# Kernel tuning notes

Hardware: AMD Instinct MI355X
Metric: run time of the kernel (lower is better)

## Reference

```python
import jax, jax.numpy as jnp
import numpy as np

B, C, REP, H, W = 4, 256, 128, 32, 128
EPS = 1e-5


def _conv1x1(x, w, b=None):
    # x: [B, Cin, H, W], w: [Cout, Cin]
    y = jnp.einsum('oc,bchw->bohw', w, x)
    if b is not None:
        y = y + b[None, :, None, None]
    return y


def _bn_train(x, gamma, beta):
    # BatchNorm2d in training mode: batch stats over (B, H, W)
    mean = jnp.mean(x, axis=(0, 2, 3), keepdims=True)
    var = jnp.var(x, axis=(0, 2, 3), keepdims=True)
    xn = (x - mean) * jax.lax.rsqrt(var + EPS)
    return gamma[None, :, None, None] * xn + beta[None, :, None, None]


def setup_inputs() -> dict:
    key = jax.random.key(0)
    ks = jax.random.split(key, 20)
    f = lambda k, s: jax.random.normal(k, s, dtype=jnp.float32)
    inp = {
        'left': f(ks[0], (B, C, H, W)),
        'right': f(ks[1], (B, C, H, W)),
        'pre_l': jax.random.uniform(ks[2], (B, 1, H, W), dtype=jnp.float32) * W,
        'pre_r': jax.random.uniform(ks[3], (B, 1, H, W), dtype=jnp.float32) * W,
        'query_l': f(ks[4], (B, REP, H, W)),
        'key_l': f(ks[5], (B, REP, H, W)),
        'query_r': f(ks[6], (B, REP, H, W)),
        'key_r': f(ks[7], (B, REP, H, W)),
        # learned 1x1-conv params (kernel stored as [Cout, Cin])
        'theta_w': f(ks[8], (REP, C + 1)) * 0.02,
        'theta_b': f(ks[9], (REP,)) * 0.02,
        'phi_w': f(ks[10], (REP, C)) * 0.02,
        'phi_b': f(ks[11], (REP,)) * 0.02,
        'g_w': f(ks[12], (REP, C)) * 0.02,
        'g_b': f(ks[13], (REP,)) * 0.02,
        'up_w': f(ks[14], (C, REP)) * 0.02,
        'up_b': f(ks[15], (C,)) * 0.02,
        'bn_gamma': f(ks[16], (C,)) * 0.1 + 1.0,
        'bn_beta': f(ks[17], (C,)) * 0.1,
    }
    return inp


def _side(x_q, x_kv, pre, query, key_feat,
          theta_w, theta_b, phi_w, phi_b, g_w, g_b,
          up_w, up_b, bn_gamma, bn_beta):
    hw = H * W
    pre = pre / W
    # theta: [B, hw, REP]
    theta = _conv1x1(jnp.concatenate([x_q, pre], axis=1), theta_w, theta_b)
    theta = theta.reshape(B, REP, hw).transpose(0, 2, 1) + \
        query.reshape(B, REP, hw).transpose(0, 2, 1)
    # phi: [B, REP, hw]
    phi = _conv1x1(x_kv, phi_w, phi_b).reshape(B, REP, hw) + \
        key_feat.reshape(B, REP, hw)
    # g: [B, hw, REP]
    g = _conv1x1(x_kv, g_w, g_b).reshape(B, REP, hw).transpose(0, 2, 1)
    # attention over all hw key positions: [B, hw, hw]
    atten = jax.nn.softmax(jnp.einsum('bqc,bck->bqk', theta, phi), axis=-1)
    # soft-argmax over key column index (arange(W) tiled H times along key axis)
    col_idx = jnp.tile(jnp.arange(W, dtype=jnp.float32), H)  # [hw]
    exp_col = jnp.einsum('bqk,k->bq', atten, col_idx)        # [B, hw]
    q_col = (jnp.arange(hw, dtype=jnp.float32) % W)[None, :]  # [1, hw]
    index = (q_col - exp_col).reshape(B, H, W)
    # value aggregation + residual projection
    after = jnp.einsum('bqk,bkc->bqc', atten, g)
    after = after.transpose(0, 2, 1).reshape(B, REP, H, W)
    out = x_q + _bn_train(_conv1x1(after, up_w, up_b), bn_gamma, bn_beta)
    return out, index


def reference(left, right, pre_l, pre_r, query_l, key_l, query_r, key_r,
              theta_w, theta_b, phi_w, phi_b, g_w, g_b,
              up_w, up_b, bn_gamma, bn_beta):
    l_n, index_l = _side(left, right, pre_l, query_l, key_r,
                         theta_w, theta_b, phi_w, phi_b, g_w, g_b,
                         up_w, up_b, bn_gamma, bn_beta)
    r_n, index_r = _side(right, left, pre_r, query_r, key_l,
                         theta_w, theta_b, phi_w, phi_b, g_w, g_b,
                         up_w, up_b, bn_gamma, bn_beta)
    return (l_n, r_n, index_l, index_r)
```

## Files before the change

### kernel.cpp

```cpp
#include <hip/hip_runtime.h>


typedef unsigned short u16;
typedef unsigned int   u32;
typedef float        floatx4 __attribute__((ext_vector_type(4)));
typedef unsigned int uintx4  __attribute__((ext_vector_type(4)));
typedef unsigned int uintx2  __attribute__((ext_vector_type(2)));
typedef _Float16     half8   __attribute__((ext_vector_type(8)));
typedef __fp16       fp16x2  __attribute__((ext_vector_type(2)));

#define HW 4096
#define CB 256
#define RP 128
#define EPSF 1e-5f

static __device__ __forceinline__ u16 f2bf(float f) {
  u32 u = __float_as_uint(f);
  u32 r = u + 0x7FFFu + ((u >> 16) & 1u);
  return (u16)(r >> 16);
}
static __device__ __forceinline__ float bf2f(u16 h) {
  return __uint_as_float(((u32)h) << 16);
}
static __device__ __forceinline__ u16 f2h(float f) {
  _Float16 h = (_Float16)f;
  return __builtin_bit_cast(u16, h);
}
static __device__ __forceinline__ float h2f(u16 h) {
  return (float)__builtin_bit_cast(_Float16, h);
}
static __device__ __forceinline__ half8 as_h8(uintx4 v) {
  return __builtin_bit_cast(half8, v);
}
static __device__ __forceinline__ u32 pkrtz(float a, float b) {
  fp16x2 h = __builtin_amdgcn_cvt_pkrtz(a, b);
  return __builtin_bit_cast(u32, h);
}
static __device__ __forceinline__ u32 pk2h(float a, float b) {
  return (u32)f2h(a) | ((u32)f2h(b) << 16);
}
static __device__ __forceinline__ void barrier_nodrain() {
  __builtin_amdgcn_sched_barrier(0);
  asm volatile("s_waitcnt lgkmcnt(0)" ::: "memory");
  __builtin_amdgcn_s_barrier();
  __builtin_amdgcn_sched_barrier(0);
}

union Pk4 { u16 u[4]; uintx2 v; };

struct ProjCfg {
  const float* x; const float* w; const float* bias;
  const float* add; const float* pre; u16* out;
  int wstride; int transposed;
};
struct ProjCfg6 { ProjCfg c[6]; };

#define XSTR 40

__global__ __launch_bounds__(256) void ra_projm(ProjCfg6 cfg)
{
  __shared__ u16 x_lds[128 * XSTR];
  __shared__ u16 w_lds[128 * XSTR];
  const ProjCfg C = cfg.c[blockIdx.x >> 7];
  const int inner = blockIdx.x & 127;
  const int b    = inner >> 5;
  const int pos0 = (inner & 31) * 128;
  const int tid  = threadIdx.x;
  const int wv   = tid >> 6;
  const int lane = tid & 63;
  const int ln16 = lane & 15;
  const int quad = lane >> 4;
  const int mbase = wv * 32;

  const int xc0 = (tid & 7) * 4, xp0 = (tid >> 3) * 4;
  const int wrr = tid >> 1, wch = (tid & 1) * 16;

  floatx4 acc[2][8];
  #pragma unroll
  for (int mt = 0; mt < 2; mt++)
    #pragma unroll
    for (int nt = 0; nt < 8; nt++) acc[mt][nt] = (floatx4)0.0f;

  #pragma unroll 1
  for (int cc = 0; cc < 8; ++cc) {
    floatx4 xr[4];
    #pragma unroll
    for (int i = 0; i < 4; i++)
      xr[i] = *(const floatx4*)(C.x + (size_t)(b * CB + cc * 32 + xc0 + i) * HW + pos0 + xp0);
    float ww[16];
    {
      const float* wp = C.w + (size_t)wrr * C.wstride + cc * 32 + wch;
      #pragma unroll
      for (int i = 0; i < 16; i++) ww[i] = wp[i];
    }
    __syncthreads();
    #pragma unroll
    for (int pp = 0; pp < 4; pp++) {
      uintx2 v;
      v[0] = pk2h(xr[0][pp], xr[1][pp]);
      v[1] = pk2h(xr[2][pp], xr[3][pp]);
      *(uintx2*)&x_lds[(xp0 + pp) * XSTR + xc0] = v;
    }
    {
      uintx4 v0, v1;
      v0[0] = pk2h(ww[0], ww[1]);  v0[1] = pk2h(ww[2], ww[3]);
      v0[2] = pk2h(ww[4], ww[5]);  v0[3] = pk2h(ww[6], ww[7]);
      v1[0] = pk2h(ww[8], ww[9]);  v1[1] = pk2h(ww[10], ww[11]);
      v1[2] = pk2h(ww[12], ww[13]); v1[3] = pk2h(ww[14], ww[15]);
      *(uintx4*)&w_lds[wrr * XSTR + wch]     = v0;
      *(uintx4*)&w_lds[wrr * XSTR + wch + 8] = v1;
    }
    __syncthreads();
    if (!C.transposed) {
      half8 a0 = as_h8(*(const uintx4*)&w_lds[(mbase + ln16) * XSTR + quad * 8]);
      half8 a1 = as_h8(*(const uintx4*)&w_lds[(mbase + 16 + ln16) * XSTR + quad * 8]);
      #pragma unroll
      for (int nt = 0; nt < 8; nt++) {
        half8 bf = as_h8(*(const uintx4*)&x_lds[(nt * 16 + ln16) * XSTR + quad * 8]);
        acc[0][nt] = __builtin_amdgcn_mfma_f32_16x16x32_f16(a0, bf, acc[0][nt], 0, 0, 0);
        acc[1][nt] = __builtin_amdgcn_mfma_f32_16x16x32_f16(a1, bf, acc[1][nt], 0, 0, 0);
      }
    } else {
      half8 a0 = as_h8(*(const uintx4*)&x_lds[(mbase + ln16) * XSTR + quad * 8]);
      half8 a1 = as_h8(*(const uintx4*)&x_lds[(mbase + 16 + ln16) * XSTR + quad * 8]);
      #pragma unroll
      for (int nt = 0; nt < 8; nt++) {
        half8 bf = as_h8(*(const uintx4*)&w_lds[(nt * 16 + ln16) * XSTR + quad * 8]);
        acc[0][nt] = __builtin_amdgcn_mfma_f32_16x16x32_f16(a0, bf, acc[0][nt], 0, 0, 0);
        acc[1][nt] = __builtin_amdgcn_mfma_f32_16x16x32_f16(a1, bf, acc[1][nt], 0, 0, 0);
      }
    }
  }

  if (!C.transposed) {
    #pragma unroll
    for (int mt = 0; mt < 2; mt++) {
      const int r0 = mbase + mt * 16 + quad * 4;
      floatx4 bi = *(const floatx4*)(C.bias + r0);
      float wc[4];
      if (C.pre) {
        #pragma unroll
        for (int rr = 0; rr < 4; rr++) wc[rr] = C.w[(size_t)(r0 + rr) * C.wstride + 256];
      }
      #pragma unroll
      for (int nt = 0; nt < 8; nt++) {
        const int pos = pos0 + nt * 16 + ln16;
        floatx4 v = acc[mt][nt];
        #pragma unroll
        for (int rr = 0; rr < 4; rr++) v[rr] += bi[rr];
        if (C.pre) {
          const float pv = C.pre[(size_t)b * HW + pos] * (1.f / 128.f);
          #pragma unroll
          for (int rr = 0; rr < 4; rr++) v[rr] += pv * wc[rr];
        }
        if (C.add) {
          #pragma unroll
          for (int rr = 0; rr < 4; rr++)
            v[rr] += C.add[(size_t)(b * RP + r0 + rr) * HW + pos];
        }
        Pk4 pk;
        #pragma unroll
        for (int rr = 0; rr < 4; rr++) pk.u[rr] = f2h(v[rr]);
        *(uintx2*)(C.out + (size_t)(b * HW + pos) * RP + r0) = pk.v;
      }
    }
  } else {
    #pragma unroll
    for (int nt = 0; nt < 8; nt++) {
      const int r = nt * 16 + ln16;
      const float bs = C.bias[r];
      #pragma unroll
      for (int mt = 0; mt < 2; mt++) {
        const int pv = pos0 + mbase + mt * 16 + quad * 4;
        floatx4 v = acc[mt][nt];
        Pk4 pk;
        #pragma unroll
        for (int rr = 0; rr < 4; rr++) pk.u[rr] = f2h(v[rr] + bs);
        *(uintx2*)(C.out + (size_t)(b * RP + r) * HW + pv) = pk.v;
      }
    }
  }
}

__global__ __launch_bounds__(256) void ra_flash(
    const u16* __restrict__ thetaL, const u16* __restrict__ phiTL,
    const u16* __restrict__ gTL,
    const u16* __restrict__ thetaR, const u16* __restrict__ phiTR,
    const u16* __restrict__ gTR,
    u16* __restrict__ afterL, u16* __restrict__ afterR,
    float* __restrict__ idxL, float* __restrict__ idxR)
{
  __shared__ uintx4 phi_lds[16 * 65];
  __shared__ uintx4 g_lds[8 * 129];
  __shared__ u16 P_lds[4][16 * 76];

  const int tid  = threadIdx.x;
  const int bx   = blockIdx.x;
  const int side = bx >> 8;
  const int sbx  = bx & 255;
  const u16* __restrict__ theta = side ? thetaR : thetaL;
  const u16* __restrict__ phiT  = side ? phiTR  : phiTL;
  const u16* __restrict__ gT    = side ? gTR    : gTL;

  const int b    = sbx >> 6;
  const int q0   = (sbx & 63) * 64;
  const int wv   = tid >> 6;
  const int lane = tid & 63;
  const int ln16 = lane & 15;
  const int quad = lane >> 4;

  uintx4 aq[4];
  {
    const uintx4* tr = (const uintx4*)(theta + (size_t)(b * HW + q0 + wv * 16 + ln16) * RP);
    #pragma unroll
    for (int c = 0; c < 4; c++) aq[c] = tr[c * 4 + quad];
  }

  half8 cf0, cf1;
  {
    #pragma unroll
    for (int i = 0; i < 8; i++) {
      float c0 = (ln16 == 0) ? (float)(quad * 8 + i)      : (ln16 == 1 ? 1.f : 0.f);
      float c1 = (ln16 == 0) ? (float)(32 + quad * 8 + i) : (ln16 == 1 ? 1.f : 0.f);
      cf0[i] = (_Float16)c0;
      cf1[i] = (_Float16)c1;
    }
  }

  floatx4 accO[8];
  #pragma unroll
  for (int v = 0; v < 8; v++) accO[v] = (floatx4)0.0f;
  floatx4 accE  = (floatx4)0.0f;
  floatx4 accEo = (floatx4)0.0f;
  float m_q = -3.0e38f;

  const int sk  = tid >> 4, scb = tid & 15;
  const int gv_ = tid >> 3, gcb = tid & 7;

  uintx4 sp[4], sg[4];
  #pragma unroll
  for (int i = 0; i < 4; i++) {
    sp[i] = *(const uintx4*)(phiT + (size_t)(b * HW + i * 16 + sk) * RP + scb * 8);
    sg[i] = *(const uintx4*)(gT + (size_t)(b * RP + i * 32 + gv_) * HW + gcb * 8);
  }

  #pragma unroll 1
  for (int j = 0; j < 64; j++) {
    #pragma unroll
    for (int i = 0; i < 4; i++) {
      phi_lds[scb * 65 + i * 16 + sk] = sp[i];
      g_lds[gcb * 129 + i * 32 + gv_] = sg[i];
    }
    if (j < 63) {
      const int k0n = (j + 1) * 64;
      #pragma unroll
      for (int i = 0; i < 4; i++) {
        sp[i] = *(const uintx4*)(phiT + (size_t)(b * HW + k0n + i * 16 + sk) * RP + scb * 8);
        sg[i] = *(const uintx4*)(gT + (size_t)(b * RP + i * 32 + gv_) * HW + k0n + gcb * 8);
      }
    }
    barrier_nodrain();

    floatx4 sf[4];
    #pragma unroll
    for (int s = 0; s < 4; s++) sf[s] = (floatx4)0.0f;
    __builtin_amdgcn_s_setprio(1);
    #pragma unroll
    for (int c = 0; c < 4; c++) {
      half8 bth = as_h8(aq[c]);
      #pragma unroll
      for (int s = 0; s < 4; s++) {
        uintx4 ap = phi_lds[(c * 4 + quad) * 65 + s * 16 + ln16];
        sf[s] = __builtin_amdgcn_mfma_f32_16x16x32_f16(as_h8(ap), bth, sf[s], 0, 0, 0);
      }
    }
    __builtin_amdgcn_s_setprio(0);

    float ms0 = fmaxf(fmaxf(sf[0][0], sf[0][1]), fmaxf(sf[0][2], sf[0][3]));
    float ms1 = fmaxf(fmaxf(sf[1][0], sf[1][1]), fmaxf(sf[1][2], sf[1][3]));
    float ms2 = fmaxf(fmaxf(sf[2][0], sf[2][1]), fmaxf(sf[2][2], sf[2][3]));
    float ms3 = fmaxf(fmaxf(sf[3][0], sf[3][1]), fmaxf(sf[3][2], sf[3][3]));
    float mx = fmaxf(fmaxf(ms0, ms1), fmaxf(ms2, ms3));
    mx = fmaxf(mx, __shfl_xor(mx, 16));
    mx = fmaxf(mx, __shfl_xor(mx, 32));
    if (__any(mx > m_q + 8.f)) {
      const float mnew  = fmaxf(m_q, mx);
      const float alpha = __expf(m_q - mnew);
      m_q = mnew;
      accE *= alpha; accEo *= alpha;
      #pragma unroll
      for (int v = 0; v < 8; v++) accO[v] *= alpha;
    }
    #pragma unroll
    for (int s = 0; s < 4; s++) {
      float p0 = __expf(sf[s][0] - m_q);
      float p1 = __expf(sf[s][1] - m_q);
      float p2 = __expf(sf[s][2] - m_q);
      float p3 = __expf(sf[s][3] - m_q);
      uintx2 pkv;
      pkv[0] = pkrtz(p0, p1);
      pkv[1] = pkrtz(p2, p3);
      *(uintx2*)&P_lds[wv][ln16 * 76 + s * 16 + quad * 4] = pkv;
    }

    half8 pb0 = as_h8(*(const uintx4*)&P_lds[wv][ln16 * 76 + quad * 8]);
    half8 pb1 = as_h8(*(const uintx4*)&P_lds[wv][ln16 * 76 + 32 + quad * 8]);
    __builtin_amdgcn_s_setprio(1);
    #pragma unroll
    for (int vt = 0; vt < 8; vt++) {
      uintx4 ag0 = g_lds[quad * 129 + vt * 16 + ln16];
      uintx4 ag1 = g_lds[(4 + quad) * 129 + vt * 16 + ln16];
      accO[vt] = __builtin_amdgcn_mfma_f32_16x16x32_f16(as_h8(ag0), pb0, accO[vt], 0, 0, 0);
      accO[vt] = __builtin_amdgcn_mfma_f32_16x16x32_f16(as_h8(ag1), pb1, accO[vt], 0, 0, 0);
    }
    if (j & 1) {
      accEo = __builtin_amdgcn_mfma_f32_16x16x32_f16(cf0, pb0, accEo, 0, 0, 0);
      accEo = __builtin_amdgcn_mfma_f32_16x16x32_f16(cf1, pb1, accEo, 0, 0, 0);
    } else {
      accE  = __builtin_amdgcn_mfma_f32_16x16x32_f16(cf0, pb0, accE, 0, 0, 0);
      accE  = __builtin_amdgcn_mfma_f32_16x16x32_f16(cf1, pb1, accE, 0, 0, 0);
    }
    __builtin_amdgcn_s_setprio(0);
    barrier_nodrain();
  }

  const float l0 = accE[1] + accEo[1];
  const float a0 = accE[0] + accEo[0] + 64.f * accEo[1];
  const float l_all  = __shfl(l0, ln16);
  const float aC_all = __shfl(a0, ln16);

  const int q = q0 + wv * 16 + ln16;
  const size_t p = (size_t)b * HW + q;
  u16* after = side ? afterR : afterL;
  u16* orow = after + p * RP;
  const float invl = 1.f / l_all;
  #pragma unroll
  for (int vt = 0; vt < 8; vt++) {
    uintx2 pkv;
    pkv[0] = pkrtz(accO[vt][0] * invl, accO[vt][1] * invl);
    pkv[1] = pkrtz(accO[vt][2] * invl, accO[vt][3] * invl);
    *(uintx2*)(orow + vt * 16 + quad * 4) = pkv;
  }
  if (quad == 0) {
    float* idx = side ? idxR : idxL;
    idx[p] = (float)(q & 127) - aC_all * invl;
  }
}

#define WSTR 136

__global__ __launch_bounds__(256) void ra_upm(
    const u16* __restrict__ afterL, const u16* __restrict__ afterR,
    const float* __restrict__ w, const float* __restrict__ bias,
    u16* __restrict__ yL, u16* __restrict__ yR)
{
  __shared__ u16 w_lds[128 * WSTR];
  const int tid  = threadIdx.x;
  const int bx   = blockIdx.x;
  const int side = bx >> 8;
  const int sbx  = bx & 255;
  const u16* __restrict__ after = side ? afterR : afterL;
  u16* __restrict__ y = side ? yR : yL;
  const int b    = sbx >> 6;
  const int pos0 = ((sbx >> 1) & 31) * 128;
  const int hc   = sbx & 1;
  const int wv   = tid >> 6;
  const int lane = tid & 63;
  const int ln16 = lane & 15;
  const int quad = lane >> 4;

  {
    const int co = tid >> 1, rh = (tid & 1) * 64;
    const float* wp = w + (size_t)(hc * 128 + co) * RP + rh;
    #pragma unroll
    for (int i = 0; i < 8; i++) {
      floatx4 f0 = *(const floatx4*)(wp + i * 8);
      floatx4 f1 = *(const floatx4*)(wp + i * 8 + 4);
      uintx4 v;
      v[0] = pk2h(f0[0], f0[1]); v[1] = pk2h(f0[2], f0[3]);
      v[2] = pk2h(f1[0], f1[1]); v[3] = pk2h(f1[2], f1[3]);
      *(uintx4*)&w_lds[co * WSTR + rh + i * 8] = v;
    }
  }
  __syncthreads();

  floatx4 acc[2][8];
  #pragma unroll
  for (int mt = 0; mt < 2; mt++)
    #pragma unroll
    for (int nt = 0; nt < 8; nt++) acc[mt][nt] = (floatx4)0.0f;

  #pragma unroll
  for (int kk = 0; kk < 4; kk++) {
    half8 a[2];
    #pragma unroll
    for (int mt = 0; mt < 2; mt++)
      a[mt] = as_h8(*(const uintx4*)(after +
          (size_t)(b * HW + pos0 + wv * 32 + mt * 16 + ln16) * RP + kk * 32 + quad * 8));
    #pragma unroll
    for (int nt = 0; nt < 8; nt++) {
      half8 bf = as_h8(*(const uintx4*)&w_lds[(nt * 16 + ln16) * WSTR + kk * 32 + quad * 8]);
      acc[0][nt] = __builtin_amdgcn_mfma_f32_16x16x32_f16(a[0], bf, acc[0][nt], 0, 0, 0);
      acc[1][nt] = __builtin_amdgcn_mfma_f32_16x16x32_f16(a[1], bf, acc[1][nt], 0, 0, 0);
    }
  }

  #pragma unroll
  for (int nt = 0; nt < 8; nt++) {
    const int co = hc * 128 + nt * 16 + ln16;
    const float bs = bias[co];
    #pragma unroll
    for (int mt = 0; mt < 2; mt++) {
      const int pv = pos0 + wv * 32 + mt * 16 + quad * 4;
      floatx4 v = acc[mt][nt];
      Pk4 pk;
      #pragma unroll
      for (int rr = 0; rr < 4; rr++) pk.u[rr] = f2bf(v[rr] + bs);
      *(uintx2*)(y + (size_t)(b * CB + co) * HW + pv) = pk.v;
    }
  }
}

__global__ __launch_bounds__(256) void ra_stats(
    const u16* __restrict__ yL, const u16* __restrict__ yR,
    float* __restrict__ stL, float* __restrict__ stR)
{
  const int side = blockIdx.x >> 8;
  const int c = blockIdx.x & 255;
  const u16* __restrict__ y = side ? yR : yL;
  float* __restrict__ stats = side ? stR : stL;
  const int tid = threadIdx.x;
  float s = 0.f, sq = 0.f;
  for (int b = 0; b < 4; b++) {
    const uintx4* row = (const uintx4*)(y + (size_t)(b * CB + c) * HW);
    #pragma unroll
    for (int t = 0; t < 2; t++) {
      uintx4 rv = row[tid + t * 256];
      #pragma unroll
      for (int k = 0; k < 4; k++) {
        float a0 = bf2f((u16)(rv[k] & 0xffffu));
        float a1 = bf2f((u16)(rv[k] >> 16));
        s += a0 + a1; sq += a0 * a0 + a1 * a1;
      }
    }
  }
  #pragma unroll
  for (int m = 1; m < 64; m <<= 1) { s += __shfl_xor(s, m); sq += __shfl_xor(sq, m); }
  __shared__ float red[8];
  const int wv = tid >> 6;
  if ((tid & 63) == 0) { red[wv * 2] = s; red[wv * 2 + 1] = sq; }
  __syncthreads();
  if (tid == 0) {
    s  = red[0] + red[2] + red[4] + red[6];
    sq = red[1] + red[3] + red[5] + red[7];
    const float mean = s * (1.f / 16384.f);
    const float var  = sq * (1.f / 16384.f) - mean * mean;
    stats[2 * c]     = mean;
    stats[2 * c + 1] = rsqrtf(var + EPSF);
  }
}

__global__ __launch_bounds__(256) void ra_fin(
    const float* __restrict__ left, const float* __restrict__ right,
    const u16* __restrict__ yL, const u16* __restrict__ yR,
    const float* __restrict__ stL, const float* __restrict__ stR,
    const float* __restrict__ gamma, const float* __restrict__ beta,
    float* __restrict__ out)
{
  const size_t e = (size_t)blockIdx.x * 256 + threadIdx.x;
  const int side = (int)(e >> 20);
  const size_t e4 = e & 1048575;
  const int c = (int)((e4 >> 10) & 255);
  const float* x = side ? right : left;
  const u16* y = side ? yR : yL;
  const float* stats = side ? stR : stL;
  const float mean = stats[2 * c], rstd = stats[2 * c + 1];
  const float ga = gamma[c], be = beta[c];
  floatx4 xv = ((const floatx4*)x)[e4];
  uintx2 yv = ((const uintx2*)y)[e4];
  float f0 = bf2f((u16)(yv[0] & 0xffffu));
  float f1 = bf2f((u16)(yv[0] >> 16));
  float f2 = bf2f((u16)(yv[1] & 0xffffu));
  float f3 = bf2f((u16)(yv[1] >> 16));
  floatx4 o;
  o[0] = xv[0] + ga * ((f0 - mean) * rstd) + be;
  o[1] = xv[1] + ga * ((f1 - mean) * rstd) + be;
  o[2] = xv[2] + ga * ((f2 - mean) * rstd) + be;
  o[3] = xv[3] + ga * ((f3 - mean) * rstd) + be;
  ((floatx4*)out)[(size_t)side * 1048576 + e4] = o;
}

extern "C" void kernel_launch(void* const* d_in, const int* in_sizes, int n_in,
                              void* d_out, int out_size, void* d_ws, size_t ws_size,
                              hipStream_t stream)
{
  const float* left    = (const float*)d_in[0];
  const float* right   = (const float*)d_in[1];
  const float* pre_l   = (const float*)d_in[2];
  const float* pre_r   = (const float*)d_in[3];
  const float* query_l = (const float*)d_in[4];
  const float* key_l   = (const float*)d_in[5];
  const float* query_r = (const float*)d_in[6];
  const float* key_r   = (const float*)d_in[7];
  const float* theta_w = (const float*)d_in[8];
  const float* theta_b = (const float*)d_in[9];
  const float* phi_w   = (const float*)d_in[10];
  const float* phi_b   = (const float*)d_in[11];
  const float* g_w     = (const float*)d_in[12];
  const float* g_b     = (const float*)d_in[13];
  const float* up_w    = (const float*)d_in[14];
  const float* up_b    = (const float*)d_in[15];
  const float* bn_g    = (const float*)d_in[16];
  const float* bn_b    = (const float*)d_in[17];
  float* out = (float*)d_out;

  char* ws = (char*)d_ws;
  const size_t SZ = (size_t)4 * HW * RP * 2;
  u16* thetaL = (u16*)(ws);
  u16* phiTL  = (u16*)(ws + 1 * SZ);
  u16* gTL    = (u16*)(ws + 2 * SZ);
  u16* thetaR = (u16*)(ws + 3 * SZ);
  u16* phiTR  = (u16*)(ws + 4 * SZ);
  u16* gTR    = (u16*)(ws + 5 * SZ);
  u16* afterL = (u16*)(ws + 6 * SZ);
  u16* afterR = (u16*)(ws + 7 * SZ);
  u16* yL     = (u16*)(ws + 8 * SZ);
  u16* yR     = (u16*)(ws + 10 * SZ);
  float* stL  = (float*)(ws + 12 * SZ);
  float* stR  = (float*)(ws + 12 * SZ + 2048);

  dim3 blk(256);
  ProjCfg6 pc;
  pc.c[0] = { left,  theta_w, theta_b, query_l, pre_l,   thetaL, 257, 0 };
  pc.c[1] = { right, phi_w,   phi_b,   key_r,   nullptr, phiTL,  256, 0 };
  pc.c[2] = { right, g_w,     g_b,     nullptr, nullptr, gTL,    256, 1 };
  pc.c[3] = { right, theta_w, theta_b, query_r, pre_r,   thetaR, 257, 0 };
  pc.c[4] = { left,  phi_w,   phi_b,   key_l,   nullptr, phiTR,  256, 0 };
  pc.c[5] = { left,  g_w,     g_b,     nullptr, nullptr, gTR,    256, 1 };
  ra_projm<<<768, blk, 0, stream>>>(pc);

  ra_flash<<<512, blk, 0, stream>>>(thetaL, phiTL, gTL, thetaR, phiTR, gTR,
                                    afterL, afterR,
                                    out + 8388608, out + 8404992);
  ra_upm<<<512, blk, 0, stream>>>(afterL, afterR, up_w, up_b, yL, yR);
  ra_stats<<<512, blk, 0, stream>>>(yL, yR, stL, stR);
  ra_fin<<<8192, blk, 0, stream>>>(left, right, yL, yR, stL, stR, bn_g, bn_b, out);

  (void)in_sizes; (void)n_in; (void)out_size; (void)ws_size;
}
```

Baseline: 318.2 us.

## Prefetch next projection chunk in registers and fuse BN stats into up-projection

The projection kernel now loads the next 32-channel chunk of input and weights into registers while the current chunk is consumed. The loads use vector reads when the weight stride is aligned, and the barriers are swapped for a variant that does not drain outstanding loads. Separately, the batch-norm sum and sum-of-squares are accumulated in the up-projection epilogue and reduced through shared memory and atomics, which removes the separate stats kernel and its re-read of y. The final kernel now computes mean and rstd from the raw sums, and a memset zeroes the stats buffer. Stats now come from fp32 values before bf16 rounding, and atomics make the summation order nondeterministic.

```diff
diff --git a/kernel.cpp b/kernel.cpp
--- a/kernel.cpp
+++ b/kernel.cpp
@@ -74,26 +74,35 @@
 
   const int xc0 = (tid & 7) * 4, xp0 = (tid >> 3) * 4;
   const int wrr = tid >> 1, wch = (tid & 1) * 16;
+  const bool walign = (C.wstride & 3) == 0;
 
   floatx4 acc[2][8];
   #pragma unroll
   for (int mt = 0; mt < 2; mt++)
     #pragma unroll
     for (int nt = 0; nt < 8; nt++) acc[mt][nt] = (floatx4)0.0f;
+
+  floatx4 xr[4];
+  floatx4 ww4[4];
+  {
+    #pragma unroll
+    for (int i = 0; i < 4; i++)
+      xr[i] = *(const floatx4*)(C.x + (size_t)(b * CB + xc0 + i) * HW + pos0 + xp0);
+    const float* wp = C.w + (size_t)wrr * C.wstride + wch;
+    if (walign) {
+      #pragma unroll
+      for (int i = 0; i < 4; i++) ww4[i] = *(const floatx4*)(wp + i * 4);
+    } else {
+      #pragma unroll
+      for (int i = 0; i < 4; i++)
+        #pragma unroll
+        for (int jj = 0; jj < 4; jj++) ww4[i][jj] = wp[i * 4 + jj];
+    }
+  }
 
   #pragma unroll 1
   for (int cc = 0; cc < 8; ++cc) {
-    floatx4 xr[4];
-    #pragma unroll
-    for (int i = 0; i < 4; i++)
-      xr[i] = *(const floatx4*)(C.x + (size_t)(b * CB + cc * 32 + xc0 + i) * HW + pos0 + xp0);
-    float ww[16];
-    {
-      const float* wp = C.w + (size_t)wrr * C.wstride + cc * 32 + wch;
-      #pragma unroll
-      for (int i = 0; i < 16; i++) ww[i] = wp[i];
-    }
-    __syncthreads();
+    barrier_nodrain();
     #pragma unroll
     for (int pp = 0; pp < 4; pp++) {
       uintx2 v;
@@ -103,14 +112,30 @@
     }
     {
       uintx4 v0, v1;
-      v0[0] = pk2h(ww[0], ww[1]);  v0[1] = pk2h(ww[2], ww[3]);
-      v0[2] = pk2h(ww[4], ww[5]);  v0[3] = pk2h(ww[6], ww[7]);
-      v1[0] = pk2h(ww[8], ww[9]);  v1[1] = pk2h(ww[10], ww[11]);
-      v1[2] = pk2h(ww[12], ww[13]); v1[3] = pk2h(ww[14], ww[15]);
+      v0[0] = pk2h(ww4[0][0], ww4[0][1]); v0[1] = pk2h(ww4[0][2], ww4[0][3]);
+      v0[2] = pk2h(ww4[1][0], ww4[1][1]); v0[3] = pk2h(ww4[1][2], ww4[1][3]);
+      v1[0] = pk2h(ww4[2][0], ww4[2][1]); v1[1] = pk2h(ww4[2][2], ww4[2][3]);
+      v1[2] = pk2h(ww4[3][0], ww4[3][1]); v1[3] = pk2h(ww4[3][2], ww4[3][3]);
       *(uintx4*)&w_lds[wrr * XSTR + wch]     = v0;
       *(uintx4*)&w_lds[wrr * XSTR + wch + 8] = v1;
     }
-    __syncthreads();
+    if (cc < 7) {
+      const int c2 = (cc + 1) * 32;
+      #pragma unroll
+      for (int i = 0; i < 4; i++)
+        xr[i] = *(const floatx4*)(C.x + (size_t)(b * CB + c2 + xc0 + i) * HW + pos0 + xp0);
+      const float* wp = C.w + (size_t)wrr * C.wstride + c2 + wch;
+      if (walign) {
+        #pragma unroll
+        for (int i = 0; i < 4; i++) ww4[i] = *(const floatx4*)(wp + i * 4);
+      } else {
+        #pragma unroll
+        for (int i = 0; i < 4; i++)
+          #pragma unroll
+          for (int jj = 0; jj < 4; jj++) ww4[i][jj] = wp[i * 4 + jj];
+      }
+    }
+    barrier_nodrain();
     if (!C.transposed) {
       half8 a0 = as_h8(*(const uintx4*)&w_lds[(mbase + ln16) * XSTR + quad * 8]);
       half8 a1 = as_h8(*(const uintx4*)&w_lds[(mbase + 16 + ln16) * XSTR + quad * 8]);
@@ -352,7 +377,8 @@
 __global__ __launch_bounds__(256) void ra_upm(
     const u16* __restrict__ afterL, const u16* __restrict__ afterR,
     const float* __restrict__ w, const float* __restrict__ bias,
-    u16* __restrict__ yL, u16* __restrict__ yR)
+    u16* __restrict__ yL, u16* __restrict__ yR,
+    float* __restrict__ stL, float* __restrict__ stR)
 {
   __shared__ u16 w_lds[128 * WSTR];
   const int tid  = threadIdx.x;
@@ -405,58 +431,45 @@
     }
   }
 
+  float s_nt[8], q_nt[8];
   #pragma unroll
   for (int nt = 0; nt < 8; nt++) {
     const int co = hc * 128 + nt * 16 + ln16;
     const float bs = bias[co];
+    float s = 0.f, sq = 0.f;
     #pragma unroll
     for (int mt = 0; mt < 2; mt++) {
       const int pv = pos0 + wv * 32 + mt * 16 + quad * 4;
       floatx4 v = acc[mt][nt];
       Pk4 pk;
       #pragma unroll
-      for (int rr = 0; rr < 4; rr++) pk.u[rr] = f2bf(v[rr] + bs);
+      for (int rr = 0; rr < 4; rr++) {
+        const float yv = v[rr] + bs;
+        s += yv; sq += yv * yv;
+        pk.u[rr] = f2bf(yv);
+      }
       *(uintx2*)(y + (size_t)(b * CB + co) * HW + pv) = pk.v;
     }
-  }
-}
-
-__global__ __launch_bounds__(256) void ra_stats(
-    const u16* __restrict__ yL, const u16* __restrict__ yR,
-    float* __restrict__ stL, float* __restrict__ stR)
-{
-  const int side = blockIdx.x >> 8;
-  const int c = blockIdx.x & 255;
-  const u16* __restrict__ y = side ? yR : yL;
-  float* __restrict__ stats = side ? stR : stL;
-  const int tid = threadIdx.x;
-  float s = 0.f, sq = 0.f;
-  for (int b = 0; b < 4; b++) {
-    const uintx4* row = (const uintx4*)(y + (size_t)(b * CB + c) * HW);
-    #pragma unroll
-    for (int t = 0; t < 2; t++) {
-      uintx4 rv = row[tid + t * 256];
-      #pragma unroll
-      for (int k = 0; k < 4; k++) {
-        float a0 = bf2f((u16)(rv[k] & 0xffffu));
-        float a1 = bf2f((u16)(rv[k] >> 16));
-        s += a0 + a1; sq += a0 * a0 + a1 * a1;
-      }
-    }
-  }
-  #pragma unroll
-  for (int m = 1; m < 64; m <<= 1) { s += __shfl_xor(s, m); sq += __shfl_xor(sq, m); }
-  __shared__ float red[8];
-  const int wv = tid >> 6;
-  if ((tid & 63) == 0) { red[wv * 2] = s; red[wv * 2 + 1] = sq; }
+    s  += __shfl_xor(s, 16);  s  += __shfl_xor(s, 32);
+    sq += __shfl_xor(sq, 16); sq += __shfl_xor(sq, 32);
+    s_nt[nt] = s; q_nt[nt] = sq;
+  }
   __syncthreads();
-  if (tid == 0) {
-    s  = red[0] + red[2] + red[4] + red[6];
-    sq = red[1] + red[3] + red[5] + red[7];
-    const float mean = s * (1.f / 16384.f);
-    const float var  = sq * (1.f / 16384.f) - mean * mean;
-    stats[2 * c]     = mean;
-    stats[2 * c + 1] = rsqrtf(var + EPSF);
+  float* scr = (float*)w_lds;
+  if (quad == 0) {
+    #pragma unroll
+    for (int nt = 0; nt < 8; nt++) {
+      scr[wv * 128 + nt * 16 + ln16]       = s_nt[nt];
+      scr[512 + wv * 128 + nt * 16 + ln16] = q_nt[nt];
+    }
+  }
+  __syncthreads();
+  if (tid < 128) {
+    const float s  = scr[tid] + scr[128 + tid] + scr[256 + tid] + scr[384 + tid];
+    const float sq = scr[512 + tid] + scr[640 + tid] + scr[768 + tid] + scr[896 + tid];
+    float* stats = side ? stR : stL;
+    atomicAdd(&stats[2 * (hc * 128 + tid)], s);
+    atomicAdd(&stats[2 * (hc * 128 + tid) + 1], sq);
   }
 }
 
@@ -474,7 +487,10 @@
   const float* x = side ? right : left;
   const u16* y = side ? yR : yL;
   const float* stats = side ? stR : stL;
-  const float mean = stats[2 * c], rstd = stats[2 * c + 1];
+  const float s = stats[2 * c], sq = stats[2 * c + 1];
+  const float mean = s * (1.f / 16384.f);
+  const float var  = sq * (1.f / 16384.f) - mean * mean;
+  const float rstd = rsqrtf(var + EPSF);
   const float ga = gamma[c], be = beta[c];
   floatx4 xv = ((const floatx4*)x)[e4];
   uintx2 yv = ((const uintx2*)y)[e4];
@@ -529,6 +545,8 @@
   float* stL  = (float*)(ws + 12 * SZ);
   float* stR  = (float*)(ws + 12 * SZ + 2048);
 
+  hipMemsetAsync(ws + 12 * SZ, 0, 4096, stream);
+
   dim3 blk(256);
   ProjCfg6 pc;
   pc.c[0] = { left,  theta_w, theta_b, query_l, pre_l,   thetaL, 257, 0 };
@@ -542,8 +560,7 @@
   ra_flash<<<512, blk, 0, stream>>>(thetaL, phiTL, gTL, thetaR, phiTR, gTR,
                                     afterL, afterR,
                                     out + 8388608, out + 8404992);
-  ra_upm<<<512, blk, 0, stream>>>(afterL, afterR, up_w, up_b, yL, yR);
-  ra_stats<<<512, blk, 0, stream>>>(yL, yR, stL, stR);
+  ra_upm<<<512, blk, 0, stream>>>(afterL, afterR, up_w, up_b, yL, yR, stL, stR);
   ra_fin<<<8192, blk, 0, stream>>>(left, right, yL, yR, stL, stR, bn_g, bn_b, out);
 
   (void)in_sizes; (void)n_in; (void)out_size; (void)ws_size;
```

Measured after the change: 315.6 us. Within noise of the previous version (-0.8%).
